# Optimization experiments

Hardware: AMD Instinct MI355X
Metric: run time of the kernel (lower is better)

Reference implementation:

```python
import jax, jax.numpy as jnp
import numpy as np

N = 200000   # residue nodes
E = 800000   # backbone edges
P = 500000   # contact pairs to score
DIN = 128    # in_channels['res']
H = 256      # hidden per layer
L = 3        # layers


def _sage(x, src, dst, Wl, Wr, b):
    # SAGEConv: mean-aggregate source-neighbor features into dst, plus root transform
    msum = jax.ops.segment_sum(x[src], dst, num_segments=N)
    deg = jax.ops.segment_sum(jnp.ones((src.shape[0],), x.dtype), dst, num_segments=N)
    m = msum / jnp.maximum(deg, 1.0)[:, None]
    return m @ Wl + x @ Wr + b


def _graphnorm(x, w, b, ms, eps=1e-5):
    # PyG GraphNorm over a single graph (batch of all zeros)
    mu = x.mean(axis=0)
    out = x - ms * mu
    var = (out * out).mean(axis=0)
    return out / jnp.sqrt(var + eps) * w + b


def setup_inputs() -> dict:
    key = jax.random.key(0)
    ks = jax.random.split(key, 40)
    s = 0.05
    inp = {
        'x_res': jax.random.normal(ks[0], (N, DIN), jnp.float32),
        'edge_index': jax.random.randint(ks[1], (2, E), 0, N),
        'contact_pred_index': jax.random.randint(ks[2], (2, P), 0, N),
    }
    dims = [DIN, H, H]
    j = 3
    for i in range(L):
        inp['Wl%d' % i] = jax.random.normal(ks[j], (dims[i], H), jnp.float32) * s; j += 1
        inp['Wr%d' % i] = jax.random.normal(ks[j], (dims[i], H), jnp.float32) * s; j += 1
        inp['bc%d' % i] = jnp.zeros((H,), jnp.float32)
        inp['gnw%d' % i] = jnp.ones((H,), jnp.float32)
        inp['gnb%d' % i] = jnp.zeros((H,), jnp.float32)
        inp['gns%d' % i] = jnp.ones((H,), jnp.float32)
    inp['dyt_alpha'] = jnp.float32(0.5)
    inp['dyt_w'] = jnp.ones((H * L,), jnp.float32)
    inp['dyt_b'] = jnp.zeros((H * L,), jnp.float32)
    XD = [512, 512]
    inp['W1'] = jax.random.normal(ks[j], (H * L, XD[0]), jnp.float32) * s; j += 1
    inp['b1'] = jnp.zeros((XD[0],), jnp.float32)
    inp['W2'] = jax.random.normal(ks[j], (XD[0], XD[1]), jnp.float32) * s; j += 1
    inp['b2'] = jnp.zeros((XD[1],), jnp.float32)
    inp['W3'] = jax.random.normal(ks[j], (XD[1], DIN), jnp.float32) * s; j += 1
    inp['b3'] = jnp.zeros((DIN,), jnp.float32)
    CD = [256, 128]
    inp['C1'] = jax.random.normal(ks[j], (2 * DIN, CD[0]), jnp.float32) * s; j += 1
    inp['c1'] = jnp.zeros((CD[0],), jnp.float32)
    inp['C2'] = jax.random.normal(ks[j], (CD[0], CD[1]), jnp.float32) * s; j += 1
    inp['c2'] = jnp.zeros((CD[1],), jnp.float32)
    inp['C3'] = jax.random.normal(ks[j], (CD[1], 1), jnp.float32) * s; j += 1
    inp['c3'] = jnp.zeros((1,), jnp.float32)
    return inp


def reference(x_res, edge_index, contact_pred_index,
              Wl0, Wr0, bc0, gnw0, gnb0, gns0,
              Wl1, Wr1, bc1, gnw1, gnb1, gns1,
              Wl2, Wr2, bc2, gnw2, gnb2, gns2,
              dyt_alpha, dyt_w, dyt_b,
              W1, b1, W2, b2, W3, b3,
              C1, c1, C2, c2, C3, c3):
    gelu = lambda v: jax.nn.gelu(v, approximate=False)
    src, dst = edge_index[0], edge_index[1]
    inz = x_res
    h = x_res
    layers = [(Wl0, Wr0, bc0, gnw0, gnb0, gns0),
              (Wl1, Wr1, bc1, gnw1, gnb1, gns1),
              (Wl2, Wr2, bc2, gnw2, gnb2, gns2)]
    outs = []
    for i, (Wl, Wr, b, gw, gb, gs) in enumerate(layers):
        prev = h
        h = gelu(_sage(h, src, dst, Wl, Wr, b))
        h = _graphnorm(h, gw, gb, gs)
        if i > 0:
            h = h + prev
        outs.append(h)
    z = jnp.concatenate(outs, axis=1)                 # JumpingKnowledge 'cat' -> [N, 3H]
    z = jnp.tanh(dyt_alpha * z) * dyt_w + dyt_b       # DynamicTanh
    z = gelu(z @ W1 + b1)
    z = gelu(z @ W2 + b2)
    z = z @ W3 + b3
    z = z + inz                                       # residual back to input features
    z = z / (jnp.linalg.norm(z, axis=1, keepdims=True) + 1e-10)
    pair = jnp.concatenate([z[contact_pred_index[0]], z[contact_pred_index[1]]], axis=1)
    e = gelu(pair @ C1 + c1)
    e = gelu(e @ C2 + c2)
    scores = (e @ C3 + c3)[:, 0]
    return jax.nn.sigmoid(scores)
```

## Files before the change

### kernel.cpp

```cpp
#include <hip/hip_runtime.h>
#include <math.h>

typedef unsigned short u16;
typedef __attribute__((ext_vector_type(8))) short short8v;
typedef __attribute__((ext_vector_type(4))) float f32x4;

__device__ __forceinline__ float geluf(float x) {
    return 0.5f * x * (1.0f + erff(x * 0.70710678118654752f));
}
__device__ __forceinline__ float bf2f(u16 u) { return __uint_as_float((unsigned)u << 16); }
__device__ __forceinline__ u16 f2bf(float f) {
    unsigned x = __float_as_uint(f);
    unsigned r = x + 0x7FFFu + ((x >> 16) & 1u);
    return (u16)(r >> 16);
}
__device__ __forceinline__ float tanhfast(float x) {
    float cx = fminf(fmaxf(x, -15.f), 15.f);
    float t = __expf(2.f * cx);
    return (t - 1.f) / (t + 1.f);
}

template<bool BF>
__device__ __forceinline__ float4 ld4(const void* base, long long elemOff) {
    if (BF) {
        ushort4 u = *(const ushort4*)((const u16*)base + elemOff);
        return make_float4(bf2f(u.x), bf2f(u.y), bf2f(u.z), bf2f(u.w));
    } else {
        return *(const float4*)((const float*)base + elemOff);
    }
}
template<bool BF>
__device__ __forceinline__ void st4(void* base, long long elemOff, float4 v) {
    if (BF) {
        ushort4 u; u.x = f2bf(v.x); u.y = f2bf(v.y); u.z = f2bf(v.z); u.w = f2bf(v.w);
        *(ushort4*)((u16*)base + elemOff) = u;
    } else {
        *(float4*)((float*)base + elemOff) = v;
    }
}

__global__ __launch_bounds__(256) void cnt_kernel(const int* __restrict__ dst, int* __restrict__ cnt, int E, int Nn) {
    int e = blockIdx.x * 256 + threadIdx.x;
    if (e < E) {
        int d = dst[e];
        if ((unsigned)d < (unsigned)Nn) atomicAdd(&cnt[d], 1);
    }
}
__global__ __launch_bounds__(256) void scan1_kernel(const int* __restrict__ cnt, int* __restrict__ rp,
                                                    int* __restrict__ bs, int n) {
    __shared__ int sh[256];
    int i = blockIdx.x * 256 + threadIdx.x;
    int v = (i < n) ? cnt[i] : 0;
    sh[threadIdx.x] = v; __syncthreads();
    for (int o = 1; o < 256; o <<= 1) {
        int t = (threadIdx.x >= o) ? sh[threadIdx.x - o] : 0;
        __syncthreads();
        sh[threadIdx.x] += t;
        __syncthreads();
    }
    if (i < n) rp[i] = sh[threadIdx.x] - v;
    if (threadIdx.x == 255) bs[blockIdx.x] = sh[255];
}
__global__ __launch_bounds__(1024) void scan2_kernel(int* __restrict__ bs, int nb) {
    __shared__ int sh[1024];
    int v = (threadIdx.x < nb) ? bs[threadIdx.x] : 0;
    sh[threadIdx.x] = v; __syncthreads();
    for (int o = 1; o < 1024; o <<= 1) {
        int t = (threadIdx.x >= o) ? sh[threadIdx.x - o] : 0;
        __syncthreads();
        sh[threadIdx.x] += t;
        __syncthreads();
    }
    if (threadIdx.x < nb) bs[threadIdx.x] = sh[threadIdx.x] - v;
}
__global__ __launch_bounds__(256) void scan3_kernel(int* __restrict__ rp, int* __restrict__ cur,
                                                    const int* __restrict__ bs, int n, int E) {
    int i = blockIdx.x * 256 + threadIdx.x;
    if (i < n) {
        int v = rp[i] + bs[blockIdx.x];
        rp[i] = v;
        cur[i] = v;
    }
    if (i == 0) rp[n] = E;
}
__global__ __launch_bounds__(256) void fill_kernel(const int* __restrict__ src, const int* __restrict__ dst,
                                                   int* __restrict__ cur, int* __restrict__ srcs, int E, int Nn) {
    int e = blockIdx.x * 256 + threadIdx.x;
    if (e >= E) return;
    int d = dst[e];
    if ((unsigned)d >= (unsigned)Nn) return;
    int s = src[e];
    if ((unsigned)s >= (unsigned)Nn) s = 0;
    int p = atomicAdd(&cur[d], 1);
    srcs[p] = s;
}

template<bool L0>
__global__ __launch_bounds__(256) void agg_csr_kernel(const void* __restrict__ X, int ldx,
    const int* __restrict__ rp, const int* __restrict__ srcs,
    u16* __restrict__ m, int c0, int rows)
{
    int lrow = blockIdx.x * 4 + (threadIdx.x >> 6);
    if (lrow >= rows) return;
    int lane = threadIdx.x & 63;
    int r = c0 + lrow;
    int b = rp[r], e = rp[r + 1];
    float inv = 1.0f / fmaxf((float)(e - b), 1.0f);
    if (L0) {
        float a0 = 0.f, a1 = 0.f, c0a = 0.f, c1a = 0.f;
        int i = b;
        for (; i + 2 <= e; i += 2) {
            int s0 = srcs[i], s1 = srcs[i + 1];
            float2 v0 = *(const float2*)((const float*)X + (long long)s0 * ldx + lane * 2);
            float2 v1 = *(const float2*)((const float*)X + (long long)s1 * ldx + lane * 2);
            a0 += v0.x; a1 += v0.y;
            c0a += v1.x; c1a += v1.y;
        }
        if (i < e) {
            int s0 = srcs[i];
            float2 v0 = *(const float2*)((const float*)X + (long long)s0 * ldx + lane * 2);
            a0 += v0.x; a1 += v0.y;
        }
        a0 += c0a; a1 += c1a;
        ushort2 o; o.x = f2bf(a0 * inv); o.y = f2bf(a1 * inv);
        *(ushort2*)(m + (long long)lrow * 128 + lane * 2) = o;
    } else {
        float a0 = 0.f, a1 = 0.f, a2 = 0.f, a3 = 0.f;
        float b0 = 0.f, b1 = 0.f, b2 = 0.f, b3 = 0.f;
        int i = b;
        for (; i + 2 <= e; i += 2) {
            int s0 = srcs[i], s1 = srcs[i + 1];
            ushort4 u0 = *(const ushort4*)((const u16*)X + (long long)s0 * ldx + lane * 4);
            ushort4 u1 = *(const ushort4*)((const u16*)X + (long long)s1 * ldx + lane * 4);
            a0 += bf2f(u0.x); a1 += bf2f(u0.y); a2 += bf2f(u0.z); a3 += bf2f(u0.w);
            b0 += bf2f(u1.x); b1 += bf2f(u1.y); b2 += bf2f(u1.z); b3 += bf2f(u1.w);
        }
        if (i < e) {
            int s0 = srcs[i];
            ushort4 u0 = *(const ushort4*)((const u16*)X + (long long)s0 * ldx + lane * 4);
            a0 += bf2f(u0.x); a1 += bf2f(u0.y); a2 += bf2f(u0.z); a3 += bf2f(u0.w);
        }
        a0 += b0; a1 += b1; a2 += b2; a3 += b3;
        ushort4 o;
        o.x = f2bf(a0 * inv); o.y = f2bf(a1 * inv); o.z = f2bf(a2 * inv); o.w = f2bf(a3 * inv);
        *(ushort4*)(m + (long long)lrow * 256 + lane * 4) = o;
    }
}

struct PrepArgs {
    const float* W[11];
    short* outp[11];
    int K[11], Nc[11], kOff[11], Ktot[11];
    int start[12];
};
__global__ __launch_bounds__(256) void prep_all_kernel(PrepArgs a) {
    int idx = blockIdx.x * 256 + threadIdx.x;
    if (idx >= a.start[11]) return;
    int si = 0;
    #pragma unroll
    for (int j = 1; j < 11; ++j) si += (idx >= a.start[j]);
    int local = idx - a.start[si];
    int Nc = a.Nc[si];
    int k = local / Nc, n = local % Nc;
    a.outp[si][(long long)n * a.Ktot[si] + a.kOff[si] + k] = (short)f2bf(a.W[si][local]);
}

template<bool BF>
__device__ __forceinline__ void loadrow(const void* base, long long off, short8v& o0, short8v& o1) {
    if (BF) {
        const short* p = (const short*)base + off;
        o0 = *(const short8v*)p;
        o1 = *(const short8v*)(p + 8);
    } else {
        const float* p = (const float*)base + off;
        float4 a = *(const float4*)p;
        float4 b = *(const float4*)(p + 4);
        float4 c = *(const float4*)(p + 8);
        float4 d = *(const float4*)(p + 12);
        short8v r0, r1;
        r0[0] = (short)f2bf(a.x); r0[1] = (short)f2bf(a.y); r0[2] = (short)f2bf(a.z); r0[3] = (short)f2bf(a.w);
        r0[4] = (short)f2bf(b.x); r0[5] = (short)f2bf(b.y); r0[6] = (short)f2bf(b.z); r0[7] = (short)f2bf(b.w);
        r1[0] = (short)f2bf(c.x); r1[1] = (short)f2bf(c.y); r1[2] = (short)f2bf(c.z); r1[3] = (short)f2bf(c.w);
        r1[4] = (short)f2bf(d.x); r1[5] = (short)f2bf(d.y); r1[6] = (short)f2bf(d.z); r1[7] = (short)f2bf(d.w);
        o0 = r0; o1 = r1;
    }
}

template<int EPI, bool GATHER, bool A1BF, bool A2BF, bool CBF>
__global__ __launch_bounds__(256) void mm_kernel(
    const void* __restrict__ A1, int lda1,
    const void* __restrict__ A2, int lda2,
    int K1, int K2,
    const short* __restrict__ Bhi, int ldb,
    const float* __restrict__ bias,
    const int* __restrict__ g1, const int* __restrict__ g2, int gmax,
    const float* __restrict__ resid, int ldres,
    void* __restrict__ C, int ldc, int M)
{
    __shared__ short As[128 * 40];
    __shared__ short Bh[128 * 40];
    const int t = threadIdx.x;
    const int rowbase = blockIdx.y * 128;
    const int colbase = blockIdx.x * 128;
    const int srow = t >> 1;
    const int sh = (t & 1) << 4;
    const int lane = t & 63;
    const int wv = t >> 6;
    const int wr = (wv >> 1) << 6;
    const int wc = (wv & 1) << 6;
    const int l15 = lane & 15;
    const int kreg = (lane >> 4) << 3;
    const int rgrp = (lane >> 4) << 2;
    f32x4 acc[4][4] = {};
    const int k1t = K1 >> 5;
    const int KT = (K1 + K2) >> 5;

    for (int kt = 0; kt < KT; ++kt) {
        const bool p1 = kt < k1t;
        {
            short8v a0 = {0,0,0,0,0,0,0,0}, a1 = {0,0,0,0,0,0,0,0};
            int r = rowbase + srow;
            if (r < M) {
                long long rr = r;
                if (GATHER) {
                    int gg = (p1 ? g1 : g2)[r];
                    if (gg < 0) gg = 0;
                    if (gg >= gmax) gg = gmax - 1;
                    rr = gg;
                }
                const int kbl = (p1 ? kt : kt - k1t) << 5;
                if (p1) loadrow<A1BF>(A1, rr * (long long)lda1 + kbl + sh, a0, a1);
                else    loadrow<A2BF>(A2, rr * (long long)lda2 + kbl + sh, a0, a1);
            }
            *(short8v*)&As[srow * 40 + sh]     = a0;
            *(short8v*)&As[srow * 40 + sh + 8] = a1;
        }
        {
            long long boff = (long long)(colbase + srow) * ldb + (kt << 5) + sh;
            *(short8v*)&Bh[srow * 40 + sh]     = *(const short8v*)(Bhi + boff);
            *(short8v*)&Bh[srow * 40 + sh + 8] = *(const short8v*)(Bhi + boff + 8);
        }
        __syncthreads();
        short8v a4[4], b4[4];
        #pragma unroll
        for (int mr = 0; mr < 4; ++mr)
            a4[mr] = *(short8v*)&As[(wr + mr * 16 + l15) * 40 + kreg];
        #pragma unroll
        for (int nr = 0; nr < 4; ++nr)
            b4[nr] = *(short8v*)&Bh[(wc + nr * 16 + l15) * 40 + kreg];
        #pragma unroll
        for (int mr = 0; mr < 4; ++mr)
            #pragma unroll
            for (int nr = 0; nr < 4; ++nr)
                acc[mr][nr] = __builtin_amdgcn_mfma_f32_16x16x32_bf16(a4[mr], b4[nr], acc[mr][nr], 0, 0, 0);
        __syncthreads();
    }

    #pragma unroll
    for (int nr = 0; nr < 4; ++nr) {
        int c = colbase + wc + nr * 16 + l15;
        float bi = bias[c];
        #pragma unroll
        for (int mr = 0; mr < 4; ++mr) {
            #pragma unroll
            for (int i = 0; i < 4; ++i) {
                int r = rowbase + wr + mr * 16 + rgrp + i;
                if (r >= M) continue;
                float v = acc[mr][nr][i] + bi;
                if (EPI == 1) v = geluf(v);
                if (EPI == 3) v += resid[(long long)r * ldres + c];
                if (CBF) ((u16*)C)[(long long)r * ldc + c] = f2bf(v);
                else     ((float*)C)[(long long)r * ldc + c] = v;
            }
        }
    }
}

__global__ __launch_bounds__(256) void colstat_kernel(const u16* __restrict__ G, int ldg, int M,
                               float* __restrict__ s1, float* __restrict__ s2) {
    int c = threadIdx.x;
    float a = 0.f, b = 0.f;
    for (int r = blockIdx.x; r < M; r += gridDim.x) {
        float v = bf2f(G[(long long)r * ldg + c]);
        a += v; b += v * v;
    }
    atomicAdd(&s1[c], a);
    atomicAdd(&s2[c], b);
}

__global__ __launch_bounds__(256) void gn_apply_kernel(u16* __restrict__ G, int ldg,
    const u16* __restrict__ prev, int ldp, int M,
    const float* __restrict__ s1, const float* __restrict__ s2,
    const float* __restrict__ gw, const float* __restrict__ gb, const float* __restrict__ gs,
    float invN)
{
    long long idx = (long long)blockIdx.x * blockDim.x + threadIdx.x;
    if (idx >= (long long)M * 64) return;
    int c0 = (int)(idx & 63) << 2;
    long long r = idx >> 6;
    float4 g = ld4<true>(G, r * ldg + c0);
    float o[4] = {g.x, g.y, g.z, g.w};
    #pragma unroll
    for (int j = 0; j < 4; ++j) {
        int c = c0 + j;
        float mu = s1[c] * invN;
        float ms = gs[c];
        float var = s2[c] * invN - mu * mu * ms * (2.0f - ms);
        float rstd = rsqrtf(var + 1e-5f);
        o[j] = (o[j] - ms * mu) * rstd * gw[c] + gb[c];
    }
    if (prev) {
        float4 pv = ld4<true>(prev, r * ldp + c0);
        o[0] += pv.x; o[1] += pv.y; o[2] += pv.z; o[3] += pv.w;
    }
    st4<true>(G, r * ldg + c0, make_float4(o[0], o[1], o[2], o[3]));
}

__global__ __launch_bounds__(256) void dyt_kernel(u16* __restrict__ Z,
    const float* __restrict__ alphaP, const float* __restrict__ w, const float* __restrict__ b,
    long long total)
{
    long long idx = (long long)blockIdx.x * blockDim.x + threadIdx.x;
    if (idx >= total) return;
    int c0 = (int)(idx % 96) << 3;
    long long r = idx / 96;
    float alpha = alphaP[0];
    short8v z = *(short8v*)(Z + r * 768 + c0);
    float4 w0 = *(const float4*)(w + c0);
    float4 w1 = *(const float4*)(w + c0 + 4);
    float4 b0 = *(const float4*)(b + c0);
    float4 b1 = *(const float4*)(b + c0 + 4);
    short8v o;
    o[0] = (short)f2bf(tanhfast(alpha * bf2f((u16)z[0])) * w0.x + b0.x);
    o[1] = (short)f2bf(tanhfast(alpha * bf2f((u16)z[1])) * w0.y + b0.y);
    o[2] = (short)f2bf(tanhfast(alpha * bf2f((u16)z[2])) * w0.z + b0.z);
    o[3] = (short)f2bf(tanhfast(alpha * bf2f((u16)z[3])) * w0.w + b0.w);
    o[4] = (short)f2bf(tanhfast(alpha * bf2f((u16)z[4])) * w1.x + b1.x);
    o[5] = (short)f2bf(tanhfast(alpha * bf2f((u16)z[5])) * w1.y + b1.y);
    o[6] = (short)f2bf(tanhfast(alpha * bf2f((u16)z[6])) * w1.z + b1.z);
    o[7] = (short)f2bf(tanhfast(alpha * bf2f((u16)z[7])) * w1.w + b1.w);
    *(short8v*)(Z + r * 768 + c0) = o;
}

__global__ __launch_bounds__(256) void norm_kernel(u16* __restrict__ zf, int M) {
    int row = (int)(((long long)blockIdx.x * blockDim.x + threadIdx.x) >> 6);
    int lane = threadIdx.x & 63;
    if (row >= M) return;
    ushort2 u = *(ushort2*)(zf + (long long)row * 128 + lane * 2);
    float vx = bf2f(u.x), vy = bf2f(u.y);
    float s = vx * vx + vy * vy;
    #pragma unroll
    for (int o = 32; o > 0; o >>= 1) s += __shfl_xor(s, o);
    float inv = 1.0f / (sqrtf(s) + 1e-10f);
    u.x = f2bf(vx * inv); u.y = f2bf(vy * inv);
    *(ushort2*)(zf + (long long)row * 128 + lane * 2) = u;
}

__global__ __launch_bounds__(256) void score_kernel(const u16* __restrict__ e2,
    const float* __restrict__ C3, const float* __restrict__ c3,
    float* __restrict__ out, int M)
{
    int row = (int)(((long long)blockIdx.x * blockDim.x + threadIdx.x) >> 6);
    int lane = threadIdx.x & 63;
    if (row >= M) return;
    ushort2 u = *(const ushort2*)(e2 + (long long)row * 128 + lane * 2);
    float2 w = *(const float2*)(C3 + lane * 2);
    float s = bf2f(u.x) * w.x + bf2f(u.y) * w.y;
    #pragma unroll
    for (int o = 32; o > 0; o >>= 1) s += __shfl_xor(s, o);
    if (lane == 0) {
        float x = s + c3[0];
        out[row] = 1.0f / (1.0f + expf(-x));
    }
}

extern "C" void kernel_launch(void* const* d_in, const int* in_sizes, int n_in,
                              void* d_out, int out_size, void* d_ws, size_t ws_size,
                              hipStream_t stream) {
    const float* x_res = (const float*)d_in[0];
    const int* eidx = (const int*)d_in[1];
    const int* cidx = (const int*)d_in[2];
    const int N = in_sizes[0] / 128;
    const int E = in_sizes[1] / 2;
    const int P = in_sizes[2] / 2;
    const int* src = eidx;
    const int* dst = eidx + E;
    const int* g1 = cidx;
    const int* g2 = cidx + P;
    const float* Wl[3] = {(const float*)d_in[3], (const float*)d_in[9],  (const float*)d_in[15]};
    const float* Wr[3] = {(const float*)d_in[4], (const float*)d_in[10], (const float*)d_in[16]};
    const float* bc[3] = {(const float*)d_in[5], (const float*)d_in[11], (const float*)d_in[17]};
    const float* gnw[3] = {(const float*)d_in[6], (const float*)d_in[12], (const float*)d_in[18]};
    const float* gnb[3] = {(const float*)d_in[7], (const float*)d_in[13], (const float*)d_in[19]};
    const float* gns[3] = {(const float*)d_in[8], (const float*)d_in[14], (const float*)d_in[20]};
    const float* alphaP = (const float*)d_in[21];
    const float* dytw = (const float*)d_in[22];
    const float* dytb = (const float*)d_in[23];
    const float* W1 = (const float*)d_in[24]; const float* b1 = (const float*)d_in[25];
    const float* W2 = (const float*)d_in[26]; const float* b2 = (const float*)d_in[27];
    const float* W3 = (const float*)d_in[28]; const float* b3 = (const float*)d_in[29];
    const float* C1 = (const float*)d_in[30]; const float* c1 = (const float*)d_in[31];
    const float* C2 = (const float*)d_in[32]; const float* c2 = (const float*)d_in[33];
    const float* C3 = (const float*)d_in[34]; const float* c3 = (const float*)d_in[35];
    float* out = (float*)d_out;

    char* ws = (char*)d_ws;
    size_t off = 0;
    size_t zOff  = off; off += (size_t)N * 768 * 2;     off = (off + 255) & ~(size_t)255;
    size_t stOff = off; off += 2048;                    off = (off + 255) & ~(size_t)255;
    size_t zfOff = off; off += (size_t)N * 128 * 2;     off = (off + 255) & ~(size_t)255;
    size_t rpOff = off; off += (size_t)(N + 1) * 4;     off = (off + 255) & ~(size_t)255;
    size_t curOff = off; off += (size_t)N * 4;          off = (off + 255) & ~(size_t)255;
    size_t srcsOff = off; off += (size_t)E * 4;         off = (off + 255) & ~(size_t)255;
    size_t bsOff = off; off += 4096;                    off = (off + 255) & ~(size_t)255;
    static const size_t se[8] = {65536, 131072, 131072, 393216, 262144, 65536, 65536, 32768};
    short* wt[8];
    for (int i = 0; i < 8; ++i) {
        wt[i] = (short*)(ws + off);
        off += 2 * se[i];
        off = (off + 255) & ~(size_t)255;
    }
    size_t pOff = off;
    size_t avail = ws_size > pOff ? ws_size - pOff : 0;

    u16*   Z    = (u16*)(ws + zOff);
    float* st   = (float*)(ws + stOff);
    u16*   zf   = (u16*)(ws + zfOff);
    int*   rp   = (int*)(ws + rpOff);
    int*   cur  = (int*)(ws + curOff);
    int*   srcs = (int*)(ws + srcsOff);
    int*   bs   = (int*)(ws + bsOff);
    u16*   pbuf = (u16*)(ws + pOff);

    int NC = (int)((avail /  512) & ~(size_t)127); if (NC < 128) NC = 128; if (NC > N) NC = N;
    int S  = (int)((avail / 2048) & ~(size_t)127); if (S  < 128) S  = 128; if (S  > N) S  = N;
    int PC = (int)((avail /  768) & ~(size_t)127); if (PC < 128) PC = 128; if (PC > P) PC = P;

    dim3 blk(256);

    {
        PrepArgs a;
        const float* Ws[11] = {Wl[0], Wr[0], Wl[1], Wr[1], Wl[2], Wr[2], W1, W2, W3, C1, C2};
        short* Os[11] = {wt[0], wt[0], wt[1], wt[1], wt[2], wt[2], wt[3], wt[4], wt[5], wt[6], wt[7]};
        int Ks[11]    = {128, 128, 256, 256, 256, 256, 768, 512, 512, 256, 256};
        int Ncs[11]   = {256, 256, 256, 256, 256, 256, 512, 512, 128, 256, 128};
        int kOffs[11] = {0, 128, 0, 256, 0, 256, 0, 0, 0, 0, 0};
        int Ktots[11] = {256, 256, 512, 512, 512, 512, 768, 512, 512, 256, 256};
        int s = 0;
        for (int i = 0; i < 11; ++i) {
            a.W[i] = Ws[i]; a.outp[i] = Os[i];
            a.K[i] = Ks[i]; a.Nc[i] = Ncs[i]; a.kOff[i] = kOffs[i]; a.Ktot[i] = Ktots[i];
            a.start[i] = s;
            s += Ks[i] * Ncs[i];
        }
        a.start[11] = s;
        prep_all_kernel<<<(s + 255) / 256, 256, 0, stream>>>(a);
    }

    int nb = (N + 255) / 256;
    hipMemsetAsync(cur, 0, (size_t)N * 4, stream);
    cnt_kernel<<<(E + 255) / 256, 256, 0, stream>>>(dst, cur, E, N);
    scan1_kernel<<<nb, 256, 0, stream>>>(cur, rp, bs, N);
    scan2_kernel<<<1, 1024, 0, stream>>>(bs, nb);
    scan3_kernel<<<nb, 256, 0, stream>>>(rp, cur, bs, N, E);
    fill_kernel<<<(E + 255) / 256, 256, 0, stream>>>(src, dst, cur, srcs, E, N);

    u16* m = pbuf;
    for (int l = 0; l < 3; ++l) {
        u16* Zl = Z + l * 256;
        for (int c0 = 0; c0 < N; c0 += NC) {
            int rows = (N - c0 < NC) ? (N - c0) : NC;
            int aggblocks = (rows + 3) / 4;
            dim3 grid(2, (rows + 127) / 128);
            if (l == 0) {
                agg_csr_kernel<true><<<aggblocks, 256, 0, stream>>>(x_res, 128, rp, srcs, m, c0, rows);
                mm_kernel<1, false, true, false, true><<<grid, blk, 0, stream>>>(
                    m, 128, x_res + (size_t)c0 * 128, 128, 128, 128,
                    wt[0], 256, bc[0],
                    nullptr, nullptr, 0, nullptr, 0,
                    Zl + (size_t)c0 * 768, 768, rows);
            } else {
                const u16* h = Z + (l - 1) * 256;
                agg_csr_kernel<false><<<aggblocks, 256, 0, stream>>>(h, 768, rp, srcs, m, c0, rows);
                mm_kernel<1, false, true, true, true><<<grid, blk, 0, stream>>>(
                    m, 256, h + (size_t)c0 * 768, 768, 256, 256,
                    wt[l], 512, bc[l],
                    nullptr, nullptr, 0, nullptr, 0,
                    Zl + (size_t)c0 * 768, 768, rows);
            }
        }
        hipMemsetAsync(st, 0, 512 * 4, stream);
        colstat_kernel<<<1024, 256, 0, stream>>>(Zl, 768, N, st, st + 256);
        const u16* prev = (l == 0) ? nullptr : (Z + (l - 1) * 256);
        gn_apply_kernel<<<(int)(((long long)N * 64 + 255) / 256), 256, 0, stream>>>(
            Zl, 768, prev, 768, N, st, st + 256, gnw[l], gnb[l], gns[l], 1.0f / (float)N);
    }

    dyt_kernel<<<(int)(((long long)N * 96 + 255) / 256), 256, 0, stream>>>(
        Z, alphaP, dytw, dytb, (long long)N * 96);

    {
        short* t1c = (short*)pbuf;
        short* t2c = t1c + (size_t)S * 512;
        for (int r0 = 0; r0 < N; r0 += S) {
            int rows = (N - r0 < S) ? (N - r0) : S;
            mm_kernel<1, false, true, true, true><<<dim3(4, (rows + 127) / 128), blk, 0, stream>>>(
                Z + (size_t)r0 * 768, 768, nullptr, 0, 768, 0,
                wt[3], 768, b1,
                nullptr, nullptr, 0, nullptr, 0, t1c, 512, rows);
            mm_kernel<1, false, true, true, true><<<dim3(4, (rows + 127) / 128), blk, 0, stream>>>(
                t1c, 512, nullptr, 0, 512, 0,
                wt[4], 512, b2,
                nullptr, nullptr, 0, nullptr, 0, t2c, 512, rows);
            mm_kernel<3, false, true, true, true><<<dim3(1, (rows + 127) / 128), blk, 0, stream>>>(
                t2c, 512, nullptr, 0, 512, 0,
                wt[5], 512, b3,
                nullptr, nullptr, 0, x_res + (size_t)r0 * 128, 128,
                zf + (size_t)r0 * 128, 128, rows);
        }
    }
    norm_kernel<<<(int)(((long long)N * 64 + 255) / 256), 256, 0, stream>>>(zf, N);

    {
        short* e1c = (short*)pbuf;
        short* e2c = e1c + (size_t)PC * 256;
        for (int p0 = 0; p0 < P; p0 += PC) {
            int rows = (P - p0 < PC) ? (P - p0) : PC;
            mm_kernel<1, true, true, true, true><<<dim3(2, (rows + 127) / 128), blk, 0, stream>>>(
                zf, 128, zf, 128, 128, 128,
                wt[6], 256, c1,
                g1 + p0, g2 + p0, N, nullptr, 0, e1c, 256, rows);
            mm_kernel<1, false, true, true, true><<<dim3(1, (rows + 127) / 128), blk, 0, stream>>>(
                e1c, 256, nullptr, 0, 256, 0,
                wt[7], 256, c2,
                nullptr, nullptr, 0, nullptr, 0, e2c, 128, rows);
            score_kernel<<<(int)(((long long)rows * 64 + 255) / 256), 256, 0, stream>>>(
                (u16*)e2c, C3, c3, out + p0, rows);
        }
    }
}
```

Before: 3.650 ms.

## Fuse graphnorm stats, row norm, DyT and pair MLP chain into GEMM epilogues

Column sum and sum-of-squares for GraphNorm now accumulate in the SAGE GEMM epilogue through shared-memory and global atomics, which removes the separate colstat pass. The L2 row normalisation is folded into the final projection GEMM, and DynamicTanh for the last layer is folded into the GraphNorm apply kernel. The whole contact scoring chain (gather, C1, GELU, C2, GELU, dot with C3, sigmoid) becomes one kernel that keeps intermediates in LDS. This avoids writing and re-reading large intermediate tensors, at the cost of more LDS use, atomic contention, and uncoalesced direct gather loads from global memory in the pair kernel.

Result: faster. 3.288 ms (-9.9%).

```diff
diff --git a/kernel.cpp b/kernel.cpp
--- a/kernel.cpp
+++ b/kernel.cpp
@@ -27,15 +27,6 @@
         return make_float4(bf2f(u.x), bf2f(u.y), bf2f(u.z), bf2f(u.w));
     } else {
         return *(const float4*)((const float*)base + elemOff);
-    }
-}
-template<bool BF>
-__device__ __forceinline__ void st4(void* base, long long elemOff, float4 v) {
-    if (BF) {
-        ushort4 u; u.x = f2bf(v.x); u.y = f2bf(v.y); u.z = f2bf(v.z); u.w = f2bf(v.w);
-        *(ushort4*)((u16*)base + elemOff) = u;
-    } else {
-        *(float4*)((float*)base + elemOff) = v;
     }
 }
 
@@ -186,19 +177,21 @@
     }
 }
 
-template<int EPI, bool GATHER, bool A1BF, bool A2BF, bool CBF>
+template<int EPI, bool A1BF, bool A2BF, bool CBF, bool STAT, bool NORM>
 __global__ __launch_bounds__(256) void mm_kernel(
     const void* __restrict__ A1, int lda1,
     const void* __restrict__ A2, int lda2,
     int K1, int K2,
     const short* __restrict__ Bhi, int ldb,
     const float* __restrict__ bias,
-    const int* __restrict__ g1, const int* __restrict__ g2, int gmax,
     const float* __restrict__ resid, int ldres,
+    float* __restrict__ s1, float* __restrict__ s2,
     void* __restrict__ C, int ldc, int M)
 {
     __shared__ short As[128 * 40];
     __shared__ short Bh[128 * 40];
+    __shared__ float cst[256];
+    __shared__ float rsq[128][2];
     const int t = threadIdx.x;
     const int rowbase = blockIdx.y * 128;
     const int colbase = blockIdx.x * 128;
@@ -211,6 +204,7 @@
     const int l15 = lane & 15;
     const int kreg = (lane >> 4) << 3;
     const int rgrp = (lane >> 4) << 2;
+    if (STAT && t < 256) cst[t] = 0.f;
     f32x4 acc[4][4] = {};
     const int k1t = K1 >> 5;
     const int KT = (K1 + K2) >> 5;
@@ -221,16 +215,9 @@
             short8v a0 = {0,0,0,0,0,0,0,0}, a1 = {0,0,0,0,0,0,0,0};
             int r = rowbase + srow;
             if (r < M) {
-                long long rr = r;
-                if (GATHER) {
-                    int gg = (p1 ? g1 : g2)[r];
-                    if (gg < 0) gg = 0;
-                    if (gg >= gmax) gg = gmax - 1;
-                    rr = gg;
-                }
                 const int kbl = (p1 ? kt : kt - k1t) << 5;
-                if (p1) loadrow<A1BF>(A1, rr * (long long)lda1 + kbl + sh, a0, a1);
-                else    loadrow<A2BF>(A2, rr * (long long)lda2 + kbl + sh, a0, a1);
+                if (p1) loadrow<A1BF>(A1, (long long)r * lda1 + kbl + sh, a0, a1);
+                else    loadrow<A2BF>(A2, (long long)r * lda2 + kbl + sh, a0, a1);
             }
             *(short8v*)&As[srow * 40 + sh]     = a0;
             *(short8v*)&As[srow * 40 + sh + 8] = a1;
@@ -256,43 +243,238 @@
         __syncthreads();
     }
 
+    if (NORM) {
+        float rs[4][4] = {};
+        #pragma unroll
+        for (int nr = 0; nr < 4; ++nr) {
+            int c = colbase + wc + nr * 16 + l15;
+            float bi = bias[c];
+            #pragma unroll
+            for (int mr = 0; mr < 4; ++mr)
+                #pragma unroll
+                for (int i = 0; i < 4; ++i) {
+                    int r = rowbase + wr + mr * 16 + rgrp + i;
+                    float v = 0.f;
+                    if (r < M) {
+                        v = acc[mr][nr][i] + bi;
+                        if (EPI == 3) v += resid[(long long)r * ldres + c];
+                        if (EPI == 1) v = geluf(v);
+                    }
+                    acc[mr][nr][i] = v;
+                    rs[mr][i] += v * v;
+                }
+        }
+        #pragma unroll
+        for (int mr = 0; mr < 4; ++mr)
+            #pragma unroll
+            for (int i = 0; i < 4; ++i) {
+                float s = rs[mr][i];
+                s += __shfl_xor(s, 1); s += __shfl_xor(s, 2);
+                s += __shfl_xor(s, 4); s += __shfl_xor(s, 8);
+                rs[mr][i] = s;
+            }
+        if (l15 == 0) {
+            #pragma unroll
+            for (int mr = 0; mr < 4; ++mr)
+                #pragma unroll
+                for (int i = 0; i < 4; ++i)
+                    rsq[wr + mr * 16 + rgrp + i][wv & 1] = rs[mr][i];
+        }
+        __syncthreads();
+        #pragma unroll
+        for (int mr = 0; mr < 4; ++mr)
+            #pragma unroll
+            for (int i = 0; i < 4; ++i) {
+                int rl = wr + mr * 16 + rgrp + i;
+                int r = rowbase + rl;
+                if (r >= M) continue;
+                float inv = 1.0f / (sqrtf(rsq[rl][0] + rsq[rl][1]) + 1e-10f);
+                #pragma unroll
+                for (int nr = 0; nr < 4; ++nr) {
+                    int c = colbase + wc + nr * 16 + l15;
+                    float v = acc[mr][nr][i] * inv;
+                    if (CBF) ((u16*)C)[(long long)r * ldc + c] = f2bf(v);
+                    else     ((float*)C)[(long long)r * ldc + c] = v;
+                }
+            }
+    } else {
+        #pragma unroll
+        for (int nr = 0; nr < 4; ++nr) {
+            int c = colbase + wc + nr * 16 + l15;
+            float bi = bias[c];
+            float cp = 0.f, cq = 0.f;
+            #pragma unroll
+            for (int mr = 0; mr < 4; ++mr)
+                #pragma unroll
+                for (int i = 0; i < 4; ++i) {
+                    int r = rowbase + wr + mr * 16 + rgrp + i;
+                    if (r >= M) continue;
+                    float v = acc[mr][nr][i] + bi;
+                    if (EPI == 1) v = geluf(v);
+                    if (EPI == 3) v += resid[(long long)r * ldres + c];
+                    if (CBF) ((u16*)C)[(long long)r * ldc + c] = f2bf(v);
+                    else     ((float*)C)[(long long)r * ldc + c] = v;
+                    if (STAT) { cp += v; cq += v * v; }
+                }
+            if (STAT) {
+                cp += __shfl_xor(cp, 16); cp += __shfl_xor(cp, 32);
+                cq += __shfl_xor(cq, 16); cq += __shfl_xor(cq, 32);
+                if (lane < 16) {
+                    int cl = wc + nr * 16 + l15;
+                    atomicAdd(&cst[cl], cp);
+                    atomicAdd(&cst[128 + cl], cq);
+                }
+            }
+        }
+        if (STAT) {
+            __syncthreads();
+            if (t < 128) {
+                atomicAdd(s1 + colbase + t, cst[t]);
+                atomicAdd(s2 + colbase + t, cst[128 + t]);
+            }
+        }
+    }
+}
+
+__global__ __launch_bounds__(256) void pair_kernel(
+    const u16* __restrict__ zf, const int* __restrict__ g1, const int* __restrict__ g2,
+    int Nn, int P,
+    const short* __restrict__ C1t, const float* __restrict__ c1,
+    const short* __restrict__ C2t, const float* __restrict__ c2,
+    const float* __restrict__ C3, const float* __restrict__ c3,
+    float* __restrict__ out)
+{
+    __shared__ short E1s[128 * 264];
+    __shared__ short Bs[128 * 40];
+    __shared__ float sc[128][2];
+    const int t = threadIdx.x;
+    const int srow = t >> 1;
+    const int sh = (t & 1) << 4;
+    const int lane = t & 63;
+    const int wv = t >> 6;
+    const int wr = (wv >> 1) << 6;
+    const int wc = (wv & 1) << 6;
+    const int l15 = lane & 15;
+    const int kreg = (lane >> 4) << 3;
+    const int rgrp = (lane >> 4) << 2;
+    const int p0 = blockIdx.x * 128;
+
+    int gidx[2][4];
+    #pragma unroll
+    for (int mr = 0; mr < 4; ++mr) {
+        int pr = p0 + wr + mr * 16 + l15;
+        int a = (pr < P) ? g1[pr] : 0;
+        if ((unsigned)a >= (unsigned)Nn) a = 0;
+        gidx[0][mr] = a;
+        int b = (pr < P) ? g2[pr] : 0;
+        if ((unsigned)b >= (unsigned)Nn) b = 0;
+        gidx[1][mr] = b;
+    }
+
+    for (int ch = 0; ch < 2; ++ch) {
+        f32x4 acc[4][4] = {};
+        for (int kt = 0; kt < 8; ++kt) {
+            long long boff = (long long)(ch * 128 + srow) * 256 + (kt << 5) + sh;
+            *(short8v*)&Bs[srow * 40 + sh]     = *(const short8v*)(C1t + boff);
+            *(short8v*)&Bs[srow * 40 + sh + 8] = *(const short8v*)(C1t + boff + 8);
+            __syncthreads();
+            int half = kt >> 2;
+            int kl = ((kt & 3) << 5) + kreg;
+            short8v a4[4], b4[4];
+            #pragma unroll
+            for (int mr = 0; mr < 4; ++mr)
+                a4[mr] = *(const short8v*)((const short*)zf + (long long)gidx[half][mr] * 128 + kl);
+            #pragma unroll
+            for (int nr = 0; nr < 4; ++nr)
+                b4[nr] = *(short8v*)&Bs[(wc + nr * 16 + l15) * 40 + kreg];
+            #pragma unroll
+            for (int mr = 0; mr < 4; ++mr)
+                #pragma unroll
+                for (int nr = 0; nr < 4; ++nr)
+                    acc[mr][nr] = __builtin_amdgcn_mfma_f32_16x16x32_bf16(a4[mr], b4[nr], acc[mr][nr], 0, 0, 0);
+            __syncthreads();
+        }
+        #pragma unroll
+        for (int nr = 0; nr < 4; ++nr) {
+            int cc = wc + nr * 16 + l15;
+            float bi = c1[ch * 128 + cc];
+            #pragma unroll
+            for (int mr = 0; mr < 4; ++mr)
+                #pragma unroll
+                for (int i = 0; i < 4; ++i) {
+                    float v = geluf(acc[mr][nr][i] + bi);
+                    E1s[(wr + mr * 16 + rgrp + i) * 264 + ch * 128 + cc] = (short)f2bf(v);
+                }
+        }
+        __syncthreads();
+    }
+
+    f32x4 acc[4][4] = {};
+    for (int kt = 0; kt < 8; ++kt) {
+        long long boff = (long long)srow * 256 + (kt << 5) + sh;
+        *(short8v*)&Bs[srow * 40 + sh]     = *(const short8v*)(C2t + boff);
+        *(short8v*)&Bs[srow * 40 + sh + 8] = *(const short8v*)(C2t + boff + 8);
+        __syncthreads();
+        short8v a4[4], b4[4];
+        #pragma unroll
+        for (int mr = 0; mr < 4; ++mr)
+            a4[mr] = *(short8v*)&E1s[(wr + mr * 16 + l15) * 264 + (kt << 5) + kreg];
+        #pragma unroll
+        for (int nr = 0; nr < 4; ++nr)
+            b4[nr] = *(short8v*)&Bs[(wc + nr * 16 + l15) * 40 + kreg];
+        #pragma unroll
+        for (int mr = 0; mr < 4; ++mr)
+            #pragma unroll
+            for (int nr = 0; nr < 4; ++nr)
+                acc[mr][nr] = __builtin_amdgcn_mfma_f32_16x16x32_bf16(a4[mr], b4[nr], acc[mr][nr], 0, 0, 0);
+        __syncthreads();
+    }
+
+    float pr_[4][4] = {};
     #pragma unroll
     for (int nr = 0; nr < 4; ++nr) {
-        int c = colbase + wc + nr * 16 + l15;
-        float bi = bias[c];
-        #pragma unroll
-        for (int mr = 0; mr < 4; ++mr) {
-            #pragma unroll
-            for (int i = 0; i < 4; ++i) {
-                int r = rowbase + wr + mr * 16 + rgrp + i;
-                if (r >= M) continue;
-                float v = acc[mr][nr][i] + bi;
-                if (EPI == 1) v = geluf(v);
-                if (EPI == 3) v += resid[(long long)r * ldres + c];
-                if (CBF) ((u16*)C)[(long long)r * ldc + c] = f2bf(v);
-                else     ((float*)C)[(long long)r * ldc + c] = v;
-            }
-        }
-    }
-}
-
-__global__ __launch_bounds__(256) void colstat_kernel(const u16* __restrict__ G, int ldg, int M,
-                               float* __restrict__ s1, float* __restrict__ s2) {
-    int c = threadIdx.x;
-    float a = 0.f, b = 0.f;
-    for (int r = blockIdx.x; r < M; r += gridDim.x) {
-        float v = bf2f(G[(long long)r * ldg + c]);
-        a += v; b += v * v;
-    }
-    atomicAdd(&s1[c], a);
-    atomicAdd(&s2[c], b);
-}
-
+        int cc = wc + nr * 16 + l15;
+        float bi = c2[cc];
+        float w3 = C3[cc];
+        #pragma unroll
+        for (int mr = 0; mr < 4; ++mr)
+            #pragma unroll
+            for (int i = 0; i < 4; ++i)
+                pr_[mr][i] += geluf(acc[mr][nr][i] + bi) * w3;
+    }
+    #pragma unroll
+    for (int mr = 0; mr < 4; ++mr)
+        #pragma unroll
+        for (int i = 0; i < 4; ++i) {
+            float s = pr_[mr][i];
+            s += __shfl_xor(s, 1); s += __shfl_xor(s, 2);
+            s += __shfl_xor(s, 4); s += __shfl_xor(s, 8);
+            pr_[mr][i] = s;
+        }
+    if (l15 == 0) {
+        #pragma unroll
+        for (int mr = 0; mr < 4; ++mr)
+            #pragma unroll
+            for (int i = 0; i < 4; ++i)
+                sc[wr + mr * 16 + rgrp + i][wv & 1] = pr_[mr][i];
+    }
+    __syncthreads();
+    if (t < 128) {
+        int p = p0 + t;
+        if (p < P) {
+            float x = sc[t][0] + sc[t][1] + c3[0];
+            out[p] = 1.0f / (1.0f + expf(-x));
+        }
+    }
+}
+
+template<bool DYT>
 __global__ __launch_bounds__(256) void gn_apply_kernel(u16* __restrict__ G, int ldg,
     const u16* __restrict__ prev, int ldp, int M,
     const float* __restrict__ s1, const float* __restrict__ s2,
     const float* __restrict__ gw, const float* __restrict__ gb, const float* __restrict__ gs,
-    float invN)
+    float invN,
+    const float* __restrict__ dA, const float* __restrict__ dW, const float* __restrict__ dB)
 {
     long long idx = (long long)blockIdx.x * blockDim.x + threadIdx.x;
     if (idx >= (long long)M * 64) return;
@@ -300,6 +482,7 @@
     long long r = idx >> 6;
     float4 g = ld4<true>(G, r * ldg + c0);
     float o[4] = {g.x, g.y, g.z, g.w};
+    float alpha = DYT ? dA[0] : 0.f;
     #pragma unroll
     for (int j = 0; j < 4; ++j) {
         int c = c0 + j;
@@ -313,17 +496,23 @@
         float4 pv = ld4<true>(prev, r * ldp + c0);
         o[0] += pv.x; o[1] += pv.y; o[2] += pv.z; o[3] += pv.w;
     }
-    st4<true>(G, r * ldg + c0, make_float4(o[0], o[1], o[2], o[3]));
-}
-
-__global__ __launch_bounds__(256) void dyt_kernel(u16* __restrict__ Z,
+    if (DYT) {
+        #pragma unroll
+        for (int j = 0; j < 4; ++j)
+            o[j] = tanhfast(alpha * o[j]) * dW[c0 + j] + dB[c0 + j];
+    }
+    ushort4 u; u.x = f2bf(o[0]); u.y = f2bf(o[1]); u.z = f2bf(o[2]); u.w = f2bf(o[3]);
+    *(ushort4*)((u16*)G + r * ldg + c0) = u;
+}
+
+__global__ __launch_bounds__(256) void dyt512_kernel(u16* __restrict__ Z,
     const float* __restrict__ alphaP, const float* __restrict__ w, const float* __restrict__ b,
     long long total)
 {
     long long idx = (long long)blockIdx.x * blockDim.x + threadIdx.x;
     if (idx >= total) return;
-    int c0 = (int)(idx % 96) << 3;
-    long long r = idx / 96;
+    int c0 = (int)(idx & 63) << 3;
+    long long r = idx >> 6;
     float alpha = alphaP[0];
     short8v z = *(short8v*)(Z + r * 768 + c0);
     float4 w0 = *(const float4*)(w + c0);
@@ -340,38 +529,6 @@
     o[6] = (short)f2bf(tanhfast(alpha * bf2f((u16)z[6])) * w1.z + b1.z);
     o[7] = (short)f2bf(tanhfast(alpha * bf2f((u16)z[7])) * w1.w + b1.w);
     *(short8v*)(Z + r * 768 + c0) = o;
-}
-
-__global__ __launch_bounds__(256) void norm_kernel(u16* __restrict__ zf, int M) {
-    int row = (int)(((long long)blockIdx.x * blockDim.x + threadIdx.x) >> 6);
-    int lane = threadIdx.x & 63;
-    if (row >= M) return;
-    ushort2 u = *(ushort2*)(zf + (long long)row * 128 + lane * 2);
-    float vx = bf2f(u.x), vy = bf2f(u.y);
-    float s = vx * vx + vy * vy;
-    #pragma unroll
-    for (int o = 32; o > 0; o >>= 1) s += __shfl_xor(s, o);
-    float inv = 1.0f / (sqrtf(s) + 1e-10f);
-    u.x = f2bf(vx * inv); u.y = f2bf(vy * inv);
-    *(ushort2*)(zf + (long long)row * 128 + lane * 2) = u;
-}
-
-__global__ __launch_bounds__(256) void score_kernel(const u16* __restrict__ e2,
-    const float* __restrict__ C3, const float* __restrict__ c3,
-    float* __restrict__ out, int M)
-{
-    int row = (int)(((long long)blockIdx.x * blockDim.x + threadIdx.x) >> 6);
-    int lane = threadIdx.x & 63;
-    if (row >= M) return;
-    ushort2 u = *(const ushort2*)(e2 + (long long)row * 128 + lane * 2);
-    float2 w = *(const float2*)(C3 + lane * 2);
-    float s = bf2f(u.x) * w.x + bf2f(u.y) * w.y;
-    #pragma unroll
-    for (int o = 32; o > 0; o >>= 1) s += __shfl_xor(s, o);
-    if (lane == 0) {
-        float x = s + c3[0];
-        out[row] = 1.0f / (1.0f + expf(-x));
-    }
 }
 
 extern "C" void kernel_launch(void* const* d_in, const int* in_sizes, int n_in,
@@ -434,7 +591,6 @@
 
     int NC = (int)((avail /  512) & ~(size_t)127); if (NC < 128) NC = 128; if (NC > N) NC = N;
     int S  = (int)((avail / 2048) & ~(size_t)127); if (S  < 128) S  = 128; if (S  > N) S  = N;
-    int PC = (int)((avail /  768) & ~(size_t)127); if (PC < 128) PC = 128; if (PC > P) PC = P;
 
     dim3 blk(256);
 
@@ -468,74 +624,59 @@
     u16* m = pbuf;
     for (int l = 0; l < 3; ++l) {
         u16* Zl = Z + l * 256;
+        hipMemsetAsync(st, 0, 512 * 4, stream);
         for (int c0 = 0; c0 < N; c0 += NC) {
             int rows = (N - c0 < NC) ? (N - c0) : NC;
             int aggblocks = (rows + 3) / 4;
             dim3 grid(2, (rows + 127) / 128);
             if (l == 0) {
                 agg_csr_kernel<true><<<aggblocks, 256, 0, stream>>>(x_res, 128, rp, srcs, m, c0, rows);
-                mm_kernel<1, false, true, false, true><<<grid, blk, 0, stream>>>(
+                mm_kernel<1, true, false, true, true, false><<<grid, blk, 0, stream>>>(
                     m, 128, x_res + (size_t)c0 * 128, 128, 128, 128,
-                    wt[0], 256, bc[0],
-                    nullptr, nullptr, 0, nullptr, 0,
+                    wt[0], 256, bc[0], nullptr, 0, st, st + 256,
                     Zl + (size_t)c0 * 768, 768, rows);
             } else {
                 const u16* h = Z + (l - 1) * 256;
                 agg_csr_kernel<false><<<aggblocks, 256, 0, stream>>>(h, 768, rp, srcs, m, c0, rows);
-                mm_kernel<1, false, true, true, true><<<grid, blk, 0, stream>>>(
+                mm_kernel<1, true, true, true, true, false><<<grid, blk, 0, stream>>>(
                     m, 256, h + (size_t)c0 * 768, 768, 256, 256,
-                    wt[l], 512, bc[l],
-                    nullptr, nullptr, 0, nullptr, 0,
+                    wt[l], 512, bc[l], nullptr, 0, st, st + 256,
                     Zl + (size_t)c0 * 768, 768, rows);
             }
         }
-        hipMemsetAsync(st, 0, 512 * 4, stream);
-        colstat_kernel<<<1024, 256, 0, stream>>>(Zl, 768, N, st, st + 256);
         const u16* prev = (l == 0) ? nullptr : (Z + (l - 1) * 256);
-        gn_apply_kernel<<<(int)(((long long)N * 64 + 255) / 256), 256, 0, stream>>>(
-            Zl, 768, prev, 768, N, st, st + 256, gnw[l], gnb[l], gns[l], 1.0f / (float)N);
-    }
-
-    dyt_kernel<<<(int)(((long long)N * 96 + 255) / 256), 256, 0, stream>>>(
-        Z, alphaP, dytw, dytb, (long long)N * 96);
+        int gnblocks = (int)(((long long)N * 64 + 255) / 256);
+        if (l == 2)
+            gn_apply_kernel<true><<<gnblocks, 256, 0, stream>>>(
+                Zl, 768, prev, 768, N, st, st + 256, gnw[l], gnb[l], gns[l], 1.0f / (float)N,
+                alphaP, dytw + 512, dytb + 512);
+        else
+            gn_apply_kernel<false><<<gnblocks, 256, 0, stream>>>(
+                Zl, 768, prev, 768, N, st, st + 256, gnw[l], gnb[l], gns[l], 1.0f / (float)N,
+                nullptr, nullptr, nullptr);
+    }
+
+    dyt512_kernel<<<(int)(((long long)N * 64 + 255) / 256), 256, 0, stream>>>(
+        Z, alphaP, dytw, dytb, (long long)N * 64);
 
     {
         short* t1c = (short*)pbuf;
         short* t2c = t1c + (size_t)S * 512;
         for (int r0 = 0; r0 < N; r0 += S) {
             int rows = (N - r0 < S) ? (N - r0) : S;
-            mm_kernel<1, false, true, true, true><<<dim3(4, (rows + 127) / 128), blk, 0, stream>>>(
+            mm_kernel<1, true, true, true, false, false><<<dim3(4, (rows + 127) / 128), blk, 0, stream>>>(
                 Z + (size_t)r0 * 768, 768, nullptr, 0, 768, 0,
-                wt[3], 768, b1,
-                nullptr, nullptr, 0, nullptr, 0, t1c, 512, rows);
-            mm_kernel<1, false, true, true, true><<<dim3(4, (rows + 127) / 128), blk, 0, stream>>>(
+                wt[3], 768, b1, nullptr, 0, nullptr, nullptr, t1c, 512, rows);
+            mm_kernel<1, true, true, true, false, false><<<dim3(4, (rows + 127) / 128), blk, 0, stream>>>(
                 t1c, 512, nullptr, 0, 512, 0,
-                wt[4], 512, b2,
-                nullptr, nullptr, 0, nullptr, 0, t2c, 512, rows);
-            mm_kernel<3, false, true, true, true><<<dim3(1, (rows + 127) / 128), blk, 0, stream>>>(
+                wt[4], 512, b2, nullptr, 0, nullptr, nullptr, t2c, 512, rows);
+            mm_kernel<3, true, true, true, false, true><<<dim3(1, (rows + 127) / 128), blk, 0, stream>>>(
                 t2c, 512, nullptr, 0, 512, 0,
-                wt[5], 512, b3,
-                nullptr, nullptr, 0, x_res + (size_t)r0 * 128, 128,
+                wt[5], 512, b3, x_res + (size_t)r0 * 128, 128, nullptr, nullptr,
                 zf + (size_t)r0 * 128, 128, rows);
         }
     }
-    norm_kernel<<<(int)(((long long)N * 64 + 255) / 256), 256, 0, stream>>>(zf, N);
-
-    {
-        short* e1c = (short*)pbuf;
-        short* e2c = e1c + (size_t)PC * 256;
-        for (int p0 = 0; p0 < P; p0 += PC) {
-            int rows = (P - p0 < PC) ? (P - p0) : PC;
-            mm_kernel<1, true, true, true, true><<<dim3(2, (rows + 127) / 128), blk, 0, stream>>>(
-                zf, 128, zf, 128, 128, 128,
-                wt[6], 256, c1,
-                g1 + p0, g2 + p0, N, nullptr, 0, e1c, 256, rows);
-            mm_kernel<1, false, true, true, true><<<dim3(1, (rows + 127) / 128), blk, 0, stream>>>(
-                e1c, 256, nullptr, 0, 256, 0,
-                wt[7], 256, c2,
-                nullptr, nullptr, 0, nullptr, 0, e2c, 128, rows);
-            score_kernel<<<(int)(((long long)rows * 64 + 255) / 256), 256, 0, stream>>>(
-                (u16*)e2c, C3, c3, out + p0, rows);
-        }
-    }
-}
+
+    pair_kernel<<<(P + 127) / 128, blk, 0, stream>>>(
+        zf, g1, g2, N, P, wt[6], c1, wt[7], c2, C3, c3, out);
+}
```
